# Optimization experiments

Hardware: AMD Instinct MI355X
Metric: run time of the kernel (lower is better)

The kernel has to match this reference:

```python
import jax, jax.numpy as jnp
import numpy as np

RBF_SIGMA = 0.5
K_CTRL = 128
BN_EPS = 1e-5


def farthest_point_sampling(points, K):
    """points: (B,N,3) -> indices (B,K) int32. Sequential FPS via lax.scan."""
    B, N, _ = points.shape
    d0 = jnp.full((B, N), jnp.inf, dtype=points.dtype)
    far0 = jnp.zeros((B,), dtype=jnp.int32)

    def step(carry, _):
        dmin, far = carry
        centroid = jnp.take_along_axis(points, far[:, None, None], axis=1)  # (B,1,3)
        d = jnp.sum((points - centroid) ** 2, axis=-1)                      # (B,N)
        dmin = jnp.minimum(dmin, d)
        far = jnp.argmax(dmin, axis=-1).astype(jnp.int32)
        return (dmin, far), far

    _, rest = jax.lax.scan(step, (d0, far0), None, length=K - 1)  # rest: (K-1,B)
    return jnp.concatenate([far0[:, None], rest.T], axis=1)       # (B,K)


def _bn_relu(h, g, b):
    # BatchNorm1d in training mode: biased batch stats over rows.
    mu = h.mean(axis=0)
    var = h.var(axis=0)
    return jax.nn.relu(g * (h - mu) * jax.lax.rsqrt(var + BN_EPS) + b)


def setup_inputs() -> dict:
    key = jax.random.key(0)
    ks = jax.random.split(key, 12)
    B, N, M, F, H = 8, 16384, 16384, 1024, 512
    inp = {
        "source_rigid_2": jax.random.normal(ks[0], (B, N, 3), jnp.float32),
        "per_point_feats": jax.random.normal(ks[1], (B, N, F), jnp.float32),
        "tgt_points": jax.random.normal(ks[2], (B, M, 3), jnp.float32),
        "tgt_point_feats": jax.random.normal(ks[3], (B, M, F), jnp.float32),
        "W1": jax.random.normal(ks[4], (2 * F, H), jnp.float32) * (1.0 / np.sqrt(2 * F)),
        "b1": jnp.zeros((H,), jnp.float32),
        "g1": jnp.ones((H,), jnp.float32),
        "beta1": jnp.zeros((H,), jnp.float32),
        "W2": jax.random.normal(ks[5], (H, H), jnp.float32) * (1.0 / np.sqrt(H)),
        "b2": jnp.zeros((H,), jnp.float32),
        "g2": jnp.ones((H,), jnp.float32),
        "beta2": jnp.zeros((H,), jnp.float32),
        "W3": jnp.zeros((H, 3), jnp.float32),   # zero-init last layer (as in torch)
        "b3": jnp.zeros((3,), jnp.float32),
    }
    return inp


def reference(source_rigid_2, per_point_feats, tgt_points, tgt_point_feats,
              W1, b1, g1, beta1, W2, b2, g2, beta2, W3, b3):
    B, N, _ = source_rigid_2.shape
    K = min(K_CTRL, N)

    # 1. FPS control point selection
    cp_idx = farthest_point_sampling(source_rigid_2, K)                     # (B,K)
    control_points = jnp.take_along_axis(source_rigid_2, cp_idx[..., None], axis=1)  # (B,K,3)
    control_feats = jnp.take_along_axis(per_point_feats, cp_idx[..., None], axis=1)  # (B,K,F)

    # 2. nearest target point per control point (squared dists; argmin == cdist argmin)
    cp2 = jnp.sum(control_points ** 2, axis=-1, keepdims=True)              # (B,K,1)
    tg2 = jnp.sum(tgt_points ** 2, axis=-1)[:, None, :]                     # (B,1,M)
    cross = jnp.einsum('bkd,bmd->bkm', control_points, tgt_points)
    nn_idx = jnp.argmin(cp2 + tg2 - 2.0 * cross, axis=-1)                   # (B,K)
    tgt_local_feats = jnp.take_along_axis(tgt_point_feats, nn_idx[..., None], axis=1)  # (B,K,F)

    # 3. displacement MLP on (B*K, 2F)
    mlp_in = jnp.concatenate([control_feats, tgt_local_feats], axis=-1).reshape(B * K, -1)
    h = _bn_relu(mlp_in @ W1 + b1, g1, beta1)
    h = _bn_relu(h @ W2 + b2, g2, beta2)
    w = (h @ W3 + b3).reshape(B, K, 3)                                      # control displacements

    # 4. RBF-softmax interpolation to all N points
    diff = source_rigid_2[:, :, None, :] - control_points[:, None, :, :]    # (B,N,K,3)
    sq_dists = jnp.sum(diff ** 2, axis=-1)                                  # (B,N,K)
    weights = jax.nn.softmax(-sq_dists / (2.0 * RBF_SIGMA ** 2), axis=-1)
    delta = jnp.einsum('bnk,bkd->bnd', weights, w)
    output = source_rigid_2 + delta
    return output, delta, control_points, w
```

## Files before the change

kernel.cpp:

```cpp
#include <hip/hip_runtime.h>
#include <hip/hip_bf16.h>

#define FPS_THREADS 1024
#define PTS_PER_THR 16
#define CONV_BLOCKS 120

typedef __attribute__((ext_vector_type(8))) short bf16x8;
typedef __attribute__((ext_vector_type(4))) float f32x4;

__device__ inline unsigned long long shfl_down_u64(unsigned long long x, int off) {
    unsigned int lo = (unsigned int)(x & 0xFFFFFFFFull);
    unsigned int hi = (unsigned int)(x >> 32);
    lo = __shfl_down(lo, off, 64);
    hi = __shfl_down(hi, off, 64);
    return (((unsigned long long)hi) << 32) | lo;
}

__device__ inline unsigned short f2bf(float x) {
    union { float f; unsigned int u; } v; v.f = x;
    unsigned int r = v.u + 0x7FFFu + ((v.u >> 16) & 1u);
    return (unsigned short)(r >> 16);
}

__device__ inline float wave_max_dpp(float v) {
    int w = __float_as_int(v);
#define DPP_MAX_STEP(ctrl, rmask)                                             \
    {                                                                         \
        int _t = __builtin_amdgcn_update_dpp(w, w, ctrl, rmask, 0xf, false);  \
        w = __float_as_int(fmaxf(__int_as_float(w), __int_as_float(_t)));     \
    }
    DPP_MAX_STEP(0x111, 0xf)
    DPP_MAX_STEP(0x112, 0xf)
    DPP_MAX_STEP(0x114, 0xf)
    DPP_MAX_STEP(0x118, 0xf)
    DPP_MAX_STEP(0x142, 0xa)
    DPP_MAX_STEP(0x143, 0xc)
#undef DPP_MAX_STEP
    return __int_as_float(__builtin_amdgcn_readlane(w, 63));
}

__global__ __launch_bounds__(FPS_THREADS) void fps_conv_kernel(
        const float* __restrict__ src, int* __restrict__ cp_idx,
        float* __restrict__ out_cp,
        const float* __restrict__ W1, const float* __restrict__ W2,
        unsigned short* __restrict__ W1t, unsigned short* __restrict__ W2t,
        float* __restrict__ stats, int N, int K) {
    const int t = threadIdx.x;
    if (blockIdx.x >= 8) {
        const int cb = blockIdx.x - 8;
        if (cb == 0) { stats[t] = 0.f; stats[t + 1024] = 0.f; }
        for (size_t idx = (size_t)cb * 1024 + t; idx < (size_t)2048 * 512;
             idx += (size_t)CONV_BLOCKS * 1024) {
            int k = (int)(idx >> 9), n = (int)(idx & 511);
            W1t[(size_t)n * 2048 + k] = f2bf(W1[idx]);
        }
        for (size_t idx = (size_t)cb * 1024 + t; idx < (size_t)512 * 512;
             idx += (size_t)CONV_BLOCKS * 1024) {
            int k = (int)(idx >> 9), n = (int)(idx & 511);
            W2t[(size_t)n * 512 + k] = f2bf(W2[idx]);
        }
        return;
    }

    const int b = blockIdx.x;
    const float* p = src + (size_t)b * N * 3;

    float px[PTS_PER_THR], py[PTS_PER_THR], pz[PTS_PER_THR], dmin[PTS_PER_THR];
#pragma unroll
    for (int i = 0; i < PTS_PER_THR; ++i) {
        int j = i * FPS_THREADS + t;
        px[i] = p[j * 3 + 0];
        py[i] = p[j * 3 + 1];
        pz[i] = p[j * 3 + 2];
        dmin[i] = __builtin_huge_valf();
    }

    __shared__ unsigned long long slot[3];
    if (t == 0) { slot[0] = 0ull; slot[1] = 0ull; slot[2] = 0ull; }
    __syncthreads();

    int far = 0;
    int cur = 0;
    for (int k = 0;; ++k) {
        const float cx = p[far * 3 + 0];
        const float cy = p[far * 3 + 1];
        const float cz = p[far * 3 + 2];
        if (t == 0) {
            cp_idx[b * K + k] = far;
            out_cp[(b * K + k) * 3 + 0] = cx;
            out_cp[(b * K + k) * 3 + 1] = cy;
            out_cp[(b * K + k) * 3 + 2] = cz;
        }
        if (k == K - 1) break;

        float tmax = -1.0f;
        int jbest = 0;
#pragma unroll
        for (int i = 0; i < PTS_PER_THR; ++i) {
            float dx = px[i] - cx, dy = py[i] - cy, dz = pz[i] - cz;
            float d = dx * dx + dy * dy + dz * dz;
            float dm = fminf(dmin[i], d);
            dmin[i] = dm;
            bool c = dm > tmax;
            tmax = c ? dm : tmax;
            jbest = c ? (i * FPS_THREADS + t) : jbest;
        }

        const float wmax = wave_max_dpp(tmax);
        if (tmax == wmax) {
            unsigned long long pk =
                (((unsigned long long)__float_as_uint(wmax)) << 32) |
                (unsigned long long)(0xFFFFFFFFu - (unsigned int)jbest);
            atomicMax(&slot[cur], pk);
        }
        const int nxt = (cur == 2) ? 0 : cur + 1;
        if (t == 0) slot[nxt] = 0ull;
        __syncthreads();
        unsigned long long bb = slot[cur];
        far = (int)(0xFFFFFFFFu - (unsigned int)(bb & 0xFFFFFFFFull));
        cur = nxt;
    }
}

__global__ __launch_bounds__(256) void nn_gather(
        const float* __restrict__ tgt, const float* __restrict__ cp,
        const int* __restrict__ cp_idx,
        const float* __restrict__ src_feats, const float* __restrict__ tgt_feats,
        unsigned short* __restrict__ mlp_b, int N, int M, int F) {
    const int bk = blockIdx.x;
    const int b = bk >> 7;
    const int t = threadIdx.x;
    const float* tp = tgt + (size_t)b * M * 3;

    const float cx = cp[bk * 3 + 0], cy = cp[bk * 3 + 1], cz = cp[bk * 3 + 2];
    const float cp2 = cx * cx + cy * cy + cz * cz;

    unsigned long long best = ~0ull;
#pragma unroll 4
    for (int m = t; m < M; m += 256) {
        float tx = tp[m * 3 + 0], ty = tp[m * 3 + 1], tz = tp[m * 3 + 2];
        float tg2 = tx * tx + ty * ty + tz * tz;
        float cross = cx * tx + cy * ty + cz * tz;
        float v = (cp2 + tg2) - 2.0f * cross;
        unsigned int fb = __float_as_uint(v);
        fb = (fb & 0x80000000u) ? ~fb : (fb | 0x80000000u);
        unsigned long long pk = (((unsigned long long)fb) << 32) | (unsigned int)m;
        best = (pk < best) ? pk : best;
    }
#pragma unroll
    for (int off = 32; off >= 1; off >>= 1) {
        unsigned long long o = shfl_down_u64(best, off);
        best = (o < best) ? o : best;
    }
    __shared__ unsigned long long red[4];
    __shared__ int snn;
    if ((t & 63) == 0) red[t >> 6] = best;
    __syncthreads();
    if (t == 0) {
        unsigned long long bb = red[0];
        for (int wv = 1; wv < 4; ++wv) bb = (red[wv] < bb) ? red[wv] : bb;
        snn = (int)(bb & 0xFFFFFFFFull);
    }
    __syncthreads();
    const int nn = snn;

    const float4* a = reinterpret_cast<const float4*>(
        src_feats + ((size_t)b * N + cp_idx[bk]) * F);
    const float4* c = reinterpret_cast<const float4*>(
        tgt_feats + ((size_t)b * M + nn) * F);
    unsigned short* o = mlp_b + (size_t)bk * 2 * F;
    float4 av = a[t];
    float4 cv = c[t];
    ushort4 a4, c4;
    a4.x = f2bf(av.x); a4.y = f2bf(av.y); a4.z = f2bf(av.z); a4.w = f2bf(av.w);
    c4.x = f2bf(cv.x); c4.y = f2bf(cv.y); c4.z = f2bf(cv.z); c4.w = f2bf(cv.w);
    *reinterpret_cast<ushort4*>(&o[t * 4]) = a4;
    *reinterpret_cast<ushort4*>(&o[F + t * 4]) = c4;
}

__global__ __launch_bounds__(256) void gemm_mfma_stats(
        const unsigned short* __restrict__ A, const unsigned short* __restrict__ Bt,
        const float* __restrict__ bias, float* __restrict__ C,
        float* __restrict__ psum, float* __restrict__ psumsq,
        int M, int N, int K) {
    __shared__ __align__(16) unsigned short As[64][72];
    __shared__ __align__(16) unsigned short Bs[64][72];
    __shared__ float sS[64], sSS[64];
    const int tid = threadIdx.x;
    const int w = tid >> 6, l = tid & 63;
    const int m0 = blockIdx.y * 64, n0 = blockIdx.x * 64;

    f32x4 acc[4];
#pragma unroll
    for (int nt = 0; nt < 4; ++nt) acc[nt] = (f32x4){0.f, 0.f, 0.f, 0.f};

    const int lr = l & 15;
    const int lg = l >> 4;

    for (int kt = 0; kt < K; kt += 64) {
        __syncthreads();
#pragma unroll
        for (int s = 0; s < 2; ++s) {
            int u = tid + s * 256;
            int row = u >> 3, kc = (u & 7) * 8;
            *reinterpret_cast<uint4*>(&As[row][kc]) =
                *reinterpret_cast<const uint4*>(&A[(size_t)(m0 + row) * K + kt + kc]);
            *reinterpret_cast<uint4*>(&Bs[row][kc]) =
                *reinterpret_cast<const uint4*>(&Bt[(size_t)(n0 + row) * K + kt + kc]);
        }
        __syncthreads();
#pragma unroll
        for (int kf = 0; kf < 2; ++kf) {
            bf16x8 af = *reinterpret_cast<const bf16x8*>(&As[w * 16 + lr][kf * 32 + lg * 8]);
#pragma unroll
            for (int nt = 0; nt < 4; ++nt) {
                bf16x8 bfr = *reinterpret_cast<const bf16x8*>(&Bs[nt * 16 + lr][kf * 32 + lg * 8]);
                acc[nt] = __builtin_amdgcn_mfma_f32_16x16x32_bf16(af, bfr, acc[nt], 0, 0, 0);
            }
        }
    }

    if (tid < 64) { sS[tid] = 0.f; sSS[tid] = 0.f; }
    __syncthreads();
#pragma unroll
    for (int nt = 0; nt < 4; ++nt) {
        const int col = n0 + nt * 16 + lr;
        const float bv = bias[col];
        float s = 0.f, ss = 0.f;
#pragma unroll
        for (int r = 0; r < 4; ++r) {
            const int row = m0 + w * 16 + lg * 4 + r;
            float v = acc[nt][r] + bv;
            C[(size_t)row * N + col] = v;
            s += v; ss += v * v;
        }
        s += __shfl_xor(s, 16, 64); ss += __shfl_xor(ss, 16, 64);
        s += __shfl_xor(s, 32, 64); ss += __shfl_xor(ss, 32, 64);
        if (lg == 0) {
            atomicAdd(&sS[nt * 16 + lr], s);
            atomicAdd(&sSS[nt * 16 + lr], ss);
        }
    }
    __syncthreads();
    if (tid < 64) {
        atomicAdd(&psum[n0 + tid], sS[tid]);
        atomicAdd(&psumsq[n0 + tid], sSS[tid]);
    }
}

__global__ __launch_bounds__(256) void bn_apply_bf16(
        const float* __restrict__ Hm, const float* __restrict__ psum,
        const float* __restrict__ psumsq, const float* __restrict__ g,
        const float* __restrict__ beta, unsigned short* __restrict__ out,
        float invM) {
    const int i = (blockIdx.x * 256 + threadIdx.x) * 4;
    float4 x = *reinterpret_cast<const float4*>(&Hm[i]);
    const int c = i & 511;
    ushort4 o4;
    float xv[4] = {x.x, x.y, x.z, x.w};
    unsigned short ov[4];
#pragma unroll
    for (int j = 0; j < 4; ++j) {
        const int col = c + j;
        const float m = psum[col] * invM;
        const float var = fmaxf(psumsq[col] * invM - m * m, 0.f);
        const float rs = rsqrtf(var + 1e-5f);
        float h = fmaxf(g[col] * (xv[j] - m) * rs + beta[col], 0.f);
        ov[j] = f2bf(h);
    }
    o4.x = ov[0]; o4.y = ov[1]; o4.z = ov[2]; o4.w = ov[3];
    *reinterpret_cast<ushort4*>(&out[i]) = o4;
}

__global__ __launch_bounds__(256) void bn_head(
        const float* __restrict__ H2, const float* __restrict__ psum,
        const float* __restrict__ psumsq, const float* __restrict__ g,
        const float* __restrict__ beta, const float* __restrict__ W3,
        const float* __restrict__ b3, float* __restrict__ w_out,
        int Ncols, float invM) {
    const int r = blockIdx.x;
    const int t = threadIdx.x;
    float a0 = 0.f, a1 = 0.f, a2 = 0.f;
    for (int c = t; c < Ncols; c += 256) {
        const float m = psum[c] * invM;
        const float var = fmaxf(psumsq[c] * invM - m * m, 0.f);
        const float rs = rsqrtf(var + 1e-5f);
        float x = H2[(size_t)r * Ncols + c];
        float h = fmaxf(g[c] * (x - m) * rs + beta[c], 0.f);
        a0 += h * W3[c * 3 + 0];
        a1 += h * W3[c * 3 + 1];
        a2 += h * W3[c * 3 + 2];
    }
#pragma unroll
    for (int off = 32; off >= 1; off >>= 1) {
        a0 += __shfl_down(a0, off, 64);
        a1 += __shfl_down(a1, off, 64);
        a2 += __shfl_down(a2, off, 64);
    }
    __shared__ float red[4][3];
    if ((t & 63) == 0) {
        red[t >> 6][0] = a0; red[t >> 6][1] = a1; red[t >> 6][2] = a2;
    }
    __syncthreads();
    if (t == 0) {
        float s0 = red[0][0] + red[1][0] + red[2][0] + red[3][0];
        float s1 = red[0][1] + red[1][1] + red[2][1] + red[3][1];
        float s2 = red[0][2] + red[1][2] + red[2][2] + red[3][2];
        w_out[r * 3 + 0] = s0 + b3[0];
        w_out[r * 3 + 1] = s1 + b3[1];
        w_out[r * 3 + 2] = s2 + b3[2];
    }
}

__global__ __launch_bounds__(256) void rbf_kernel(
        const float* __restrict__ src, const float* __restrict__ cp,
        const float* __restrict__ w, float* __restrict__ outp,
        float* __restrict__ delta, int N, int K) {
    __shared__ float scx[128], scy[128], scz[128];
    __shared__ float swx[128], swy[128], swz[128];
    const int b = blockIdx.x >> 6;
    const int chunk = blockIdx.x & 63;
    const int t = threadIdx.x;
    if (t < K) {
        const int base = (b * K + t) * 3;
        scx[t] = cp[base + 0]; scy[t] = cp[base + 1]; scz[t] = cp[base + 2];
        swx[t] = w[base + 0];  swy[t] = w[base + 1];  swz[t] = w[base + 2];
    }
    __syncthreads();

    const int n = chunk * 256 + t;
    const size_t pbase = ((size_t)b * N + n) * 3;
    const float x = src[pbase + 0], y = src[pbase + 1], z = src[pbase + 2];

    float mind = __builtin_huge_valf();
    for (int k = 0; k < K; ++k) {
        float dx = x - scx[k], dy = y - scy[k], dz = z - scz[k];
        float d2 = dx * dx + dy * dy + dz * dz;
        mind = fminf(mind, d2);
    }
    float sum = 0.f, ax = 0.f, ay = 0.f, az = 0.f;
    for (int k = 0; k < K; ++k) {
        float dx = x - scx[k], dy = y - scy[k], dz = z - scz[k];
        float d2 = dx * dx + dy * dy + dz * dz;
        float e = __expf(2.0f * (mind - d2));
        sum += e;
        ax += e * swx[k]; ay += e * swy[k]; az += e * swz[k];
    }
    const float inv = 1.0f / sum;
    ax *= inv; ay *= inv; az *= inv;
    delta[pbase + 0] = ax; delta[pbase + 1] = ay; delta[pbase + 2] = az;
    outp[pbase + 0] = x + ax; outp[pbase + 1] = y + ay; outp[pbase + 2] = z + az;
}

extern "C" void kernel_launch(void* const* d_in, const int* in_sizes, int n_in,
                              void* d_out, int out_size, void* d_ws, size_t ws_size,
                              hipStream_t stream) {
    const int B = 8, N = 16384, M = 16384, F = 1024, H = 512, K = 128;
    const int BK = B * K;

    const float* src       = (const float*)d_in[0];
    const float* ppf       = (const float*)d_in[1];
    const float* tgt       = (const float*)d_in[2];
    const float* tpf       = (const float*)d_in[3];
    const float* W1        = (const float*)d_in[4];
    const float* b1        = (const float*)d_in[5];
    const float* g1        = (const float*)d_in[6];
    const float* beta1     = (const float*)d_in[7];
    const float* W2        = (const float*)d_in[8];
    const float* b2        = (const float*)d_in[9];
    const float* g2        = (const float*)d_in[10];
    const float* beta2     = (const float*)d_in[11];
    const float* W3        = (const float*)d_in[12];
    const float* b3        = (const float*)d_in[13];

    float* out_output = (float*)d_out;
    float* out_delta  = out_output + (size_t)B * N * 3;
    float* out_cp     = out_delta + (size_t)B * N * 3;
    float* out_w      = out_cp + (size_t)B * K * 3;

    char* ws = (char*)d_ws;
    int*            cp_idx = (int*)(ws + 0);
    float*          stats  = (float*)(ws + 4096);
    float* psum1   = stats;
    float* psumsq1 = stats + 512;
    float* psum2   = stats + 1024;
    float* psumsq2 = stats + 1536;
    unsigned short* mlp_b  = (unsigned short*)(ws + 16384);
    unsigned short* W1t    = (unsigned short*)(ws + 4210688);
    unsigned short* W2t    = (unsigned short*)(ws + 6307840);
    float*          h1     = (float*)(ws + 6832128);
    unsigned short* h1b    = (unsigned short*)(ws + 8929280);
    float*          h2     = (float*)(ws + 9977856);

    fps_conv_kernel<<<8 + CONV_BLOCKS, FPS_THREADS, 0, stream>>>(
        src, cp_idx, out_cp, W1, W2, W1t, W2t, stats, N, K);
    nn_gather<<<BK, 256, 0, stream>>>(tgt, out_cp, cp_idx, ppf, tpf, mlp_b, N, M, F);
    gemm_mfma_stats<<<dim3(H / 64, BK / 64), 256, 0, stream>>>(
        mlp_b, W1t, b1, h1, psum1, psumsq1, BK, H, 2 * F);
    bn_apply_bf16<<<(BK * H / 4) / 256, 256, 0, stream>>>(
        h1, psum1, psumsq1, g1, beta1, h1b, 1.0f / BK);
    gemm_mfma_stats<<<dim3(H / 64, BK / 64), 256, 0, stream>>>(
        h1b, W2t, b2, h2, psum2, psumsq2, BK, H, H);
    bn_head<<<BK, 256, 0, stream>>>(
        h2, psum2, psumsq2, g2, beta2, W3, b3, out_w, H, 1.0f / BK);
    rbf_kernel<<<B * (N / 256), 256, 0, stream>>>(src, out_cp, out_w, out_output, out_delta, N, K);
}
```

Before: 322.8 us.

## Fuse post-FPS stages into persistent mega-kernel with grid barriers; pack FPS math

Merges the nearest-neighbour gather, both GEMMs, the BN apply, the BN head and the RBF interpolation into one persistent kernel of 512 blocks. Stages are separated by atomic-counter grid barriers, which replaces five kernel launches and their gaps. The FPS kernel drops to 512 threads, with each thread holding 32 points as float2 pairs so the distance math can use packed arithmetic. The risks are idle blocks during the 128-block GEMM phases, and deadlock if all 512 blocks are not co-resident. The FPS loop also carries more serial work per thread.

```diff
diff --git a/kernel.cpp b/kernel.cpp
--- a/kernel.cpp
+++ b/kernel.cpp
@@ -1,12 +1,14 @@
 #include <hip/hip_runtime.h>
 #include <hip/hip_bf16.h>
 
-#define FPS_THREADS 1024
-#define PTS_PER_THR 16
+#define FPS_THREADS 512
+#define PAIRS_PER_THR 16
 #define CONV_BLOCKS 120
+#define MEGA_BLOCKS 512
 
 typedef __attribute__((ext_vector_type(8))) short bf16x8;
 typedef __attribute__((ext_vector_type(4))) float f32x4;
+typedef __attribute__((ext_vector_type(2))) float f32x2;
 
 __device__ inline unsigned long long shfl_down_u64(unsigned long long x, int off) {
     unsigned int lo = (unsigned int)(x & 0xFFFFFFFFull);
@@ -39,23 +41,38 @@
     return __int_as_float(__builtin_amdgcn_readlane(w, 63));
 }
 
+__device__ __forceinline__ void grid_barrier(int* c, int target) {
+    __threadfence();
+    __syncthreads();
+    if (threadIdx.x == 0) {
+        __hip_atomic_fetch_add(c, 1, __ATOMIC_ACQ_REL, __HIP_MEMORY_SCOPE_AGENT);
+        while (__hip_atomic_load(c, __ATOMIC_ACQUIRE, __HIP_MEMORY_SCOPE_AGENT) < target)
+            __builtin_amdgcn_s_sleep(1);
+    }
+    __syncthreads();
+}
+
 __global__ __launch_bounds__(FPS_THREADS) void fps_conv_kernel(
         const float* __restrict__ src, int* __restrict__ cp_idx,
         float* __restrict__ out_cp,
         const float* __restrict__ W1, const float* __restrict__ W2,
         unsigned short* __restrict__ W1t, unsigned short* __restrict__ W2t,
-        float* __restrict__ stats, int N, int K) {
+        float* __restrict__ stats, int* __restrict__ ctr, int N, int K) {
     const int t = threadIdx.x;
     if (blockIdx.x >= 8) {
         const int cb = blockIdx.x - 8;
-        if (cb == 0) { stats[t] = 0.f; stats[t + 1024] = 0.f; }
-        for (size_t idx = (size_t)cb * 1024 + t; idx < (size_t)2048 * 512;
-             idx += (size_t)CONV_BLOCKS * 1024) {
+        if (cb == 0) {
+            stats[t] = 0.f; stats[t + 512] = 0.f;
+            stats[t + 1024] = 0.f; stats[t + 1536] = 0.f;
+            if (t < 8) ctr[t] = 0;
+        }
+        for (size_t idx = (size_t)cb * FPS_THREADS + t; idx < (size_t)2048 * 512;
+             idx += (size_t)CONV_BLOCKS * FPS_THREADS) {
             int k = (int)(idx >> 9), n = (int)(idx & 511);
             W1t[(size_t)n * 2048 + k] = f2bf(W1[idx]);
         }
-        for (size_t idx = (size_t)cb * 1024 + t; idx < (size_t)512 * 512;
-             idx += (size_t)CONV_BLOCKS * 1024) {
+        for (size_t idx = (size_t)cb * FPS_THREADS + t; idx < (size_t)512 * 512;
+             idx += (size_t)CONV_BLOCKS * FPS_THREADS) {
             int k = (int)(idx >> 9), n = (int)(idx & 511);
             W2t[(size_t)n * 512 + k] = f2bf(W2[idx]);
         }
@@ -65,14 +82,15 @@
     const int b = blockIdx.x;
     const float* p = src + (size_t)b * N * 3;
 
-    float px[PTS_PER_THR], py[PTS_PER_THR], pz[PTS_PER_THR], dmin[PTS_PER_THR];
-#pragma unroll
-    for (int i = 0; i < PTS_PER_THR; ++i) {
-        int j = i * FPS_THREADS + t;
-        px[i] = p[j * 3 + 0];
-        py[i] = p[j * 3 + 1];
-        pz[i] = p[j * 3 + 2];
-        dmin[i] = __builtin_huge_valf();
+    f32x2 px2[PAIRS_PER_THR], py2[PAIRS_PER_THR], pz2[PAIRS_PER_THR], dm2[PAIRS_PER_THR];
+#pragma unroll
+    for (int a = 0; a < PAIRS_PER_THR; ++a) {
+        int j0 = (2 * a) * FPS_THREADS + t;
+        int j1 = (2 * a + 1) * FPS_THREADS + t;
+        px2[a] = (f32x2){p[j0 * 3 + 0], p[j1 * 3 + 0]};
+        py2[a] = (f32x2){p[j0 * 3 + 1], p[j1 * 3 + 1]};
+        pz2[a] = (f32x2){p[j0 * 3 + 2], p[j1 * 3 + 2]};
+        dm2[a] = (f32x2){__builtin_huge_valf(), __builtin_huge_valf()};
     }
 
     __shared__ unsigned long long slot[3];
@@ -93,17 +111,34 @@
         }
         if (k == K - 1) break;
 
+        const f32x2 vcx = (f32x2){cx, cx};
+        const f32x2 vcy = (f32x2){cy, cy};
+        const f32x2 vcz = (f32x2){cz, cz};
+
+#pragma unroll
+        for (int a = 0; a < PAIRS_PER_THR; ++a) {
+            f32x2 dx = px2[a] - vcx;
+            f32x2 dy = py2[a] - vcy;
+            f32x2 dz = pz2[a] - vcz;
+            f32x2 d = dx * dx;
+            d += dy * dy;
+            d += dz * dz;
+            f32x2 dm = dm2[a];
+            dm.x = fminf(dm.x, d.x);
+            dm.y = fminf(dm.y, d.y);
+            dm2[a] = dm;
+        }
         float tmax = -1.0f;
         int jbest = 0;
 #pragma unroll
-        for (int i = 0; i < PTS_PER_THR; ++i) {
-            float dx = px[i] - cx, dy = py[i] - cy, dz = pz[i] - cz;
-            float d = dx * dx + dy * dy + dz * dz;
-            float dm = fminf(dmin[i], d);
-            dmin[i] = dm;
-            bool c = dm > tmax;
-            tmax = c ? dm : tmax;
-            jbest = c ? (i * FPS_THREADS + t) : jbest;
+        for (int a = 0; a < PAIRS_PER_THR; ++a) {
+            f32x2 dm = dm2[a];
+            bool c0 = dm.x > tmax;
+            tmax = c0 ? dm.x : tmax;
+            jbest = c0 ? ((2 * a) * FPS_THREADS + t) : jbest;
+            bool c1 = dm.y > tmax;
+            tmax = c1 ? dm.y : tmax;
+            jbest = c1 ? ((2 * a + 1) * FPS_THREADS + t) : jbest;
         }
 
         const float wmax = wave_max_dpp(tmax);
@@ -122,73 +157,15 @@
     }
 }
 
-__global__ __launch_bounds__(256) void nn_gather(
-        const float* __restrict__ tgt, const float* __restrict__ cp,
-        const int* __restrict__ cp_idx,
-        const float* __restrict__ src_feats, const float* __restrict__ tgt_feats,
-        unsigned short* __restrict__ mlp_b, int N, int M, int F) {
-    const int bk = blockIdx.x;
-    const int b = bk >> 7;
-    const int t = threadIdx.x;
-    const float* tp = tgt + (size_t)b * M * 3;
-
-    const float cx = cp[bk * 3 + 0], cy = cp[bk * 3 + 1], cz = cp[bk * 3 + 2];
-    const float cp2 = cx * cx + cy * cy + cz * cz;
-
-    unsigned long long best = ~0ull;
-#pragma unroll 4
-    for (int m = t; m < M; m += 256) {
-        float tx = tp[m * 3 + 0], ty = tp[m * 3 + 1], tz = tp[m * 3 + 2];
-        float tg2 = tx * tx + ty * ty + tz * tz;
-        float cross = cx * tx + cy * ty + cz * tz;
-        float v = (cp2 + tg2) - 2.0f * cross;
-        unsigned int fb = __float_as_uint(v);
-        fb = (fb & 0x80000000u) ? ~fb : (fb | 0x80000000u);
-        unsigned long long pk = (((unsigned long long)fb) << 32) | (unsigned int)m;
-        best = (pk < best) ? pk : best;
-    }
-#pragma unroll
-    for (int off = 32; off >= 1; off >>= 1) {
-        unsigned long long o = shfl_down_u64(best, off);
-        best = (o < best) ? o : best;
-    }
-    __shared__ unsigned long long red[4];
-    __shared__ int snn;
-    if ((t & 63) == 0) red[t >> 6] = best;
-    __syncthreads();
-    if (t == 0) {
-        unsigned long long bb = red[0];
-        for (int wv = 1; wv < 4; ++wv) bb = (red[wv] < bb) ? red[wv] : bb;
-        snn = (int)(bb & 0xFFFFFFFFull);
-    }
-    __syncthreads();
-    const int nn = snn;
-
-    const float4* a = reinterpret_cast<const float4*>(
-        src_feats + ((size_t)b * N + cp_idx[bk]) * F);
-    const float4* c = reinterpret_cast<const float4*>(
-        tgt_feats + ((size_t)b * M + nn) * F);
-    unsigned short* o = mlp_b + (size_t)bk * 2 * F;
-    float4 av = a[t];
-    float4 cv = c[t];
-    ushort4 a4, c4;
-    a4.x = f2bf(av.x); a4.y = f2bf(av.y); a4.z = f2bf(av.z); a4.w = f2bf(av.w);
-    c4.x = f2bf(cv.x); c4.y = f2bf(cv.y); c4.z = f2bf(cv.z); c4.w = f2bf(cv.w);
-    *reinterpret_cast<ushort4*>(&o[t * 4]) = a4;
-    *reinterpret_cast<ushort4*>(&o[F + t * 4]) = c4;
-}
-
-__global__ __launch_bounds__(256) void gemm_mfma_stats(
+__device__ __forceinline__ void gemm_unit(
         const unsigned short* __restrict__ A, const unsigned short* __restrict__ Bt,
         const float* __restrict__ bias, float* __restrict__ C,
         float* __restrict__ psum, float* __restrict__ psumsq,
-        int M, int N, int K) {
-    __shared__ __align__(16) unsigned short As[64][72];
-    __shared__ __align__(16) unsigned short Bs[64][72];
-    __shared__ float sS[64], sSS[64];
+        int N, int K, int m0, int n0,
+        unsigned short (&As)[64][72], unsigned short (&Bs)[64][72],
+        float (&sS)[64], float (&sSS)[64]) {
     const int tid = threadIdx.x;
     const int w = tid >> 6, l = tid & 63;
-    const int m0 = blockIdx.y * 64, n0 = blockIdx.x * 64;
 
     f32x4 acc[4];
 #pragma unroll
@@ -248,115 +225,191 @@
     }
 }
 
-__global__ __launch_bounds__(256) void bn_apply_bf16(
-        const float* __restrict__ Hm, const float* __restrict__ psum,
-        const float* __restrict__ psumsq, const float* __restrict__ g,
-        const float* __restrict__ beta, unsigned short* __restrict__ out,
-        float invM) {
-    const int i = (blockIdx.x * 256 + threadIdx.x) * 4;
-    float4 x = *reinterpret_cast<const float4*>(&Hm[i]);
-    const int c = i & 511;
-    ushort4 o4;
-    float xv[4] = {x.x, x.y, x.z, x.w};
-    unsigned short ov[4];
-#pragma unroll
-    for (int j = 0; j < 4; ++j) {
-        const int col = c + j;
-        const float m = psum[col] * invM;
-        const float var = fmaxf(psumsq[col] * invM - m * m, 0.f);
-        const float rs = rsqrtf(var + 1e-5f);
-        float h = fmaxf(g[col] * (xv[j] - m) * rs + beta[col], 0.f);
-        ov[j] = f2bf(h);
-    }
-    o4.x = ov[0]; o4.y = ov[1]; o4.z = ov[2]; o4.w = ov[3];
-    *reinterpret_cast<ushort4*>(&out[i]) = o4;
-}
-
-__global__ __launch_bounds__(256) void bn_head(
-        const float* __restrict__ H2, const float* __restrict__ psum,
-        const float* __restrict__ psumsq, const float* __restrict__ g,
-        const float* __restrict__ beta, const float* __restrict__ W3,
-        const float* __restrict__ b3, float* __restrict__ w_out,
-        int Ncols, float invM) {
-    const int r = blockIdx.x;
+__global__ __launch_bounds__(256) void mega_kernel(
+        const float* __restrict__ src, const float* __restrict__ tgt,
+        const float* __restrict__ cp, const int* __restrict__ cp_idx,
+        const float* __restrict__ src_feats, const float* __restrict__ tgt_feats,
+        unsigned short* __restrict__ mlp_b,
+        unsigned short* __restrict__ W1t, unsigned short* __restrict__ W2t,
+        const float* __restrict__ b1, const float* __restrict__ g1, const float* __restrict__ beta1,
+        const float* __restrict__ b2, const float* __restrict__ g2, const float* __restrict__ beta2,
+        const float* __restrict__ W3, const float* __restrict__ b3,
+        float* __restrict__ h1, unsigned short* __restrict__ h1b, float* __restrict__ h2,
+        float* __restrict__ stats, int* __restrict__ ctr,
+        float* __restrict__ out_w, float* __restrict__ outp, float* __restrict__ delta,
+        int N, int M, int F, int Hc) {
+    __shared__ __align__(16) unsigned short As[64][72];
+    __shared__ __align__(16) unsigned short Bs[64][72];
+    __shared__ float sS[64], sSS[64];
+    __shared__ unsigned long long redu[4];
+    __shared__ int snn;
+    __shared__ float redh[4][3];
+    __shared__ float scx[128], scy[128], scz[128], swx[128], swy[128], swz[128];
+
+    const int blk = blockIdx.x;
     const int t = threadIdx.x;
-    float a0 = 0.f, a1 = 0.f, a2 = 0.f;
-    for (int c = t; c < Ncols; c += 256) {
-        const float m = psum[c] * invM;
-        const float var = fmaxf(psumsq[c] * invM - m * m, 0.f);
-        const float rs = rsqrtf(var + 1e-5f);
-        float x = H2[(size_t)r * Ncols + c];
-        float h = fmaxf(g[c] * (x - m) * rs + beta[c], 0.f);
-        a0 += h * W3[c * 3 + 0];
-        a1 += h * W3[c * 3 + 1];
-        a2 += h * W3[c * 3 + 2];
-    }
-#pragma unroll
-    for (int off = 32; off >= 1; off >>= 1) {
-        a0 += __shfl_down(a0, off, 64);
-        a1 += __shfl_down(a1, off, 64);
-        a2 += __shfl_down(a2, off, 64);
-    }
-    __shared__ float red[4][3];
-    if ((t & 63) == 0) {
-        red[t >> 6][0] = a0; red[t >> 6][1] = a1; red[t >> 6][2] = a2;
-    }
-    __syncthreads();
-    if (t == 0) {
-        float s0 = red[0][0] + red[1][0] + red[2][0] + red[3][0];
-        float s1 = red[0][1] + red[1][1] + red[2][1] + red[3][1];
-        float s2 = red[0][2] + red[1][2] + red[2][2] + red[3][2];
-        w_out[r * 3 + 0] = s0 + b3[0];
-        w_out[r * 3 + 1] = s1 + b3[1];
-        w_out[r * 3 + 2] = s2 + b3[2];
-    }
-}
-
-__global__ __launch_bounds__(256) void rbf_kernel(
-        const float* __restrict__ src, const float* __restrict__ cp,
-        const float* __restrict__ w, float* __restrict__ outp,
-        float* __restrict__ delta, int N, int K) {
-    __shared__ float scx[128], scy[128], scz[128];
-    __shared__ float swx[128], swy[128], swz[128];
-    const int b = blockIdx.x >> 6;
-    const int chunk = blockIdx.x & 63;
-    const int t = threadIdx.x;
-    if (t < K) {
-        const int base = (b * K + t) * 3;
-        scx[t] = cp[base + 0]; scy[t] = cp[base + 1]; scz[t] = cp[base + 2];
-        swx[t] = w[base + 0];  swy[t] = w[base + 1];  swz[t] = w[base + 2];
-    }
-    __syncthreads();
-
-    const int n = chunk * 256 + t;
-    const size_t pbase = ((size_t)b * N + n) * 3;
-    const float x = src[pbase + 0], y = src[pbase + 1], z = src[pbase + 2];
-
-    float mind = __builtin_huge_valf();
-    for (int k = 0; k < K; ++k) {
-        float dx = x - scx[k], dy = y - scy[k], dz = z - scz[k];
-        float d2 = dx * dx + dy * dy + dz * dz;
-        mind = fminf(mind, d2);
-    }
-    float sum = 0.f, ax = 0.f, ay = 0.f, az = 0.f;
-    for (int k = 0; k < K; ++k) {
-        float dx = x - scx[k], dy = y - scy[k], dz = z - scz[k];
-        float d2 = dx * dx + dy * dy + dz * dz;
-        float e = __expf(2.0f * (mind - d2));
-        sum += e;
-        ax += e * swx[k]; ay += e * swy[k]; az += e * swz[k];
-    }
-    const float inv = 1.0f / sum;
-    ax *= inv; ay *= inv; az *= inv;
-    delta[pbase + 0] = ax; delta[pbase + 1] = ay; delta[pbase + 2] = az;
-    outp[pbase + 0] = x + ax; outp[pbase + 1] = y + ay; outp[pbase + 2] = z + az;
+    float* psum1 = stats;
+    float* psumsq1 = stats + 512;
+    float* psum2 = stats + 1024;
+    float* psumsq2 = stats + 1536;
+    const float invM = 1.0f / 1024.0f;
+
+    for (int half = 0; half < 2; ++half) {
+        const int bk = blk + half * 512;
+        const int b = bk >> 7;
+        const float* tp = tgt + (size_t)b * M * 3;
+        const float cx = cp[bk * 3 + 0], cy = cp[bk * 3 + 1], cz = cp[bk * 3 + 2];
+        const float cp2 = cx * cx + cy * cy + cz * cz;
+
+        unsigned long long best = ~0ull;
+#pragma unroll 4
+        for (int m = t; m < M; m += 256) {
+            float tx = tp[m * 3 + 0], ty = tp[m * 3 + 1], tz = tp[m * 3 + 2];
+            float tg2 = tx * tx + ty * ty + tz * tz;
+            float cross = cx * tx + cy * ty + cz * tz;
+            float v = (cp2 + tg2) - 2.0f * cross;
+            unsigned int fb = __float_as_uint(v);
+            fb = (fb & 0x80000000u) ? ~fb : (fb | 0x80000000u);
+            unsigned long long pk = (((unsigned long long)fb) << 32) | (unsigned int)m;
+            best = (pk < best) ? pk : best;
+        }
+#pragma unroll
+        for (int off = 32; off >= 1; off >>= 1) {
+            unsigned long long o = shfl_down_u64(best, off);
+            best = (o < best) ? o : best;
+        }
+        if ((t & 63) == 0) redu[t >> 6] = best;
+        __syncthreads();
+        if (t == 0) {
+            unsigned long long bb = redu[0];
+            for (int wv = 1; wv < 4; ++wv) bb = (redu[wv] < bb) ? redu[wv] : bb;
+            snn = (int)(bb & 0xFFFFFFFFull);
+        }
+        __syncthreads();
+        const int nn = snn;
+
+        const float4* a4p = reinterpret_cast<const float4*>(
+            src_feats + ((size_t)b * N + cp_idx[bk]) * F);
+        const float4* c4p = reinterpret_cast<const float4*>(
+            tgt_feats + ((size_t)b * M + nn) * F);
+        unsigned short* o = mlp_b + (size_t)bk * 2 * F;
+        float4 av = a4p[t];
+        float4 cv = c4p[t];
+        ushort4 a4, c4;
+        a4.x = f2bf(av.x); a4.y = f2bf(av.y); a4.z = f2bf(av.z); a4.w = f2bf(av.w);
+        c4.x = f2bf(cv.x); c4.y = f2bf(cv.y); c4.z = f2bf(cv.z); c4.w = f2bf(cv.w);
+        *reinterpret_cast<ushort4*>(&o[t * 4]) = a4;
+        *reinterpret_cast<ushort4*>(&o[F + t * 4]) = c4;
+        __syncthreads();
+    }
+    grid_barrier(&ctr[0], MEGA_BLOCKS);
+
+    if (blk < 128) {
+        gemm_unit(mlp_b, W1t, b1, h1, psum1, psumsq1,
+                  Hc, 2 * F, (blk >> 3) * 64, (blk & 7) * 64, As, Bs, sS, sSS);
+    }
+    grid_barrier(&ctr[1], MEGA_BLOCKS);
+
+    {
+        const int i = (blk * 256 + t) * 4;
+        float4 x = *reinterpret_cast<const float4*>(&h1[i]);
+        const int c = i & 511;
+        float xv[4] = {x.x, x.y, x.z, x.w};
+        unsigned short ov[4];
+#pragma unroll
+        for (int j = 0; j < 4; ++j) {
+            const int col = c + j;
+            const float m = psum1[col] * invM;
+            const float var = fmaxf(psumsq1[col] * invM - m * m, 0.f);
+            const float rs = rsqrtf(var + 1e-5f);
+            float h = fmaxf(g1[col] * (xv[j] - m) * rs + beta1[col], 0.f);
+            ov[j] = f2bf(h);
+        }
+        ushort4 o4; o4.x = ov[0]; o4.y = ov[1]; o4.z = ov[2]; o4.w = ov[3];
+        *reinterpret_cast<ushort4*>(&h1b[i]) = o4;
+    }
+    grid_barrier(&ctr[2], MEGA_BLOCKS);
+
+    if (blk < 128) {
+        gemm_unit(h1b, W2t, b2, h2, psum2, psumsq2,
+                  Hc, Hc, (blk >> 3) * 64, (blk & 7) * 64, As, Bs, sS, sSS);
+    }
+    grid_barrier(&ctr[3], MEGA_BLOCKS);
+
+    for (int half = 0; half < 2; ++half) {
+        const int r = blk + half * 512;
+        float a0 = 0.f, a1 = 0.f, a2 = 0.f;
+        for (int c = t; c < Hc; c += 256) {
+            const float m = psum2[c] * invM;
+            const float var = fmaxf(psumsq2[c] * invM - m * m, 0.f);
+            const float rs = rsqrtf(var + 1e-5f);
+            float x = h2[(size_t)r * Hc + c];
+            float h = fmaxf(g2[c] * (x - m) * rs + beta2[c], 0.f);
+            a0 += h * W3[c * 3 + 0];
+            a1 += h * W3[c * 3 + 1];
+            a2 += h * W3[c * 3 + 2];
+        }
+#pragma unroll
+        for (int off = 32; off >= 1; off >>= 1) {
+            a0 += __shfl_down(a0, off, 64);
+            a1 += __shfl_down(a1, off, 64);
+            a2 += __shfl_down(a2, off, 64);
+        }
+        if ((t & 63) == 0) {
+            redh[t >> 6][0] = a0; redh[t >> 6][1] = a1; redh[t >> 6][2] = a2;
+        }
+        __syncthreads();
+        if (t == 0) {
+            float s0 = redh[0][0] + redh[1][0] + redh[2][0] + redh[3][0];
+            float s1 = redh[0][1] + redh[1][1] + redh[2][1] + redh[3][1];
+            float s2 = redh[0][2] + redh[1][2] + redh[2][2] + redh[3][2];
+            out_w[r * 3 + 0] = s0 + b3[0];
+            out_w[r * 3 + 1] = s1 + b3[1];
+            out_w[r * 3 + 2] = s2 + b3[2];
+        }
+        __syncthreads();
+    }
+    grid_barrier(&ctr[4], MEGA_BLOCKS);
+
+    {
+        const int b = blk >> 6;
+        const int chunk = blk & 63;
+        if (t < 128) {
+            const int base = (b * 128 + t) * 3;
+            scx[t] = cp[base + 0]; scy[t] = cp[base + 1]; scz[t] = cp[base + 2];
+            swx[t] = out_w[base + 0]; swy[t] = out_w[base + 1]; swz[t] = out_w[base + 2];
+        }
+        __syncthreads();
+
+        const int n = chunk * 256 + t;
+        const size_t pbase = ((size_t)b * N + n) * 3;
+        const float x = src[pbase + 0], y = src[pbase + 1], z = src[pbase + 2];
+
+        float mind = __builtin_huge_valf();
+        for (int k = 0; k < 128; ++k) {
+            float dx = x - scx[k], dy = y - scy[k], dz = z - scz[k];
+            float d2 = dx * dx + dy * dy + dz * dz;
+            mind = fminf(mind, d2);
+        }
+        float sum = 0.f, ax = 0.f, ay = 0.f, az = 0.f;
+        for (int k = 0; k < 128; ++k) {
+            float dx = x - scx[k], dy = y - scy[k], dz = z - scz[k];
+            float d2 = dx * dx + dy * dy + dz * dz;
+            float e = __expf(2.0f * (mind - d2));
+            sum += e;
+            ax += e * swx[k]; ay += e * swy[k]; az += e * swz[k];
+        }
+        const float inv = 1.0f / sum;
+        ax *= inv; ay *= inv; az *= inv;
+        delta[pbase + 0] = ax; delta[pbase + 1] = ay; delta[pbase + 2] = az;
+        outp[pbase + 0] = x + ax; outp[pbase + 1] = y + ay; outp[pbase + 2] = z + az;
+    }
 }
 
 extern "C" void kernel_launch(void* const* d_in, const int* in_sizes, int n_in,
                               void* d_out, int out_size, void* d_ws, size_t ws_size,
                               hipStream_t stream) {
     const int B = 8, N = 16384, M = 16384, F = 1024, H = 512, K = 128;
-    const int BK = B * K;
 
     const float* src       = (const float*)d_in[0];
     const float* ppf       = (const float*)d_in[1];
@@ -381,10 +434,7 @@
     char* ws = (char*)d_ws;
     int*            cp_idx = (int*)(ws + 0);
     float*          stats  = (float*)(ws + 4096);
-    float* psum1   = stats;
-    float* psumsq1 = stats + 512;
-    float* psum2   = stats + 1024;
-    float* psumsq2 = stats + 1536;
+    int*            ctr    = (int*)(ws + 12288);
     unsigned short* mlp_b  = (unsigned short*)(ws + 16384);
     unsigned short* W1t    = (unsigned short*)(ws + 4210688);
     unsigned short* W2t    = (unsigned short*)(ws + 6307840);
@@ -393,15 +443,10 @@
     float*          h2     = (float*)(ws + 9977856);
 
     fps_conv_kernel<<<8 + CONV_BLOCKS, FPS_THREADS, 0, stream>>>(
-        src, cp_idx, out_cp, W1, W2, W1t, W2t, stats, N, K);
-    nn_gather<<<BK, 256, 0, stream>>>(tgt, out_cp, cp_idx, ppf, tpf, mlp_b, N, M, F);
-    gemm_mfma_stats<<<dim3(H / 64, BK / 64), 256, 0, stream>>>(
-        mlp_b, W1t, b1, h1, psum1, psumsq1, BK, H, 2 * F);
-    bn_apply_bf16<<<(BK * H / 4) / 256, 256, 0, stream>>>(
-        h1, psum1, psumsq1, g1, beta1, h1b, 1.0f / BK);
-    gemm_mfma_stats<<<dim3(H / 64, BK / 64), 256, 0, stream>>>(
-        h1b, W2t, b2, h2, psum2, psumsq2, BK, H, H);
-    bn_head<<<BK, 256, 0, stream>>>(
-        h2, psum2, psumsq2, g2, beta2, W3, b3, out_w, H, 1.0f / BK);
-    rbf_kernel<<<B * (N / 256), 256, 0, stream>>>(src, out_cp, out_w, out_output, out_delta, N, K);
-}
+        src, cp_idx, out_cp, W1, W2, W1t, W2t, stats, ctr, N, K);
+    mega_kernel<<<MEGA_BLOCKS, 256, 0, stream>>>(
+        src, tgt, out_cp, cp_idx, ppf, tpf, mlp_b, W1t, W2t,
+        b1, g1, beta1, b2, g2, beta2, W3, b3,
+        h1, h1b, h2, stats, ctr, out_w, out_output, out_delta,
+        N, M, F, H);
+}
```

New measurement: 712.3 us. 2.21x slower.
